# Kernel optimization log

Measured on AMD Instinct MI355X. Metric: run time of the kernel, lower is better.

## Reference

```python
import jax, jax.numpy as jnp
import numpy as np
import math

L = 32            # one_side_length; seq_len = L*L = 1024
EMBED = 768
NDIM = 16
N_SSM = 768
DIRS = 4
K = DIRS * N_SSM  # kernel_dim = 3072
REPEAT = EMBED // N_SSM
SCALE = math.sqrt(1.0 / NDIM)


def _compute_kernel(A_angle, A_radius, B1p, B2p, C1p, C2p):
    # Polar-parameterized complex diagonal A's (4 transition coeffs), sigmoid B, raw C.
    ang = jax.nn.sigmoid(A_angle) * (2.0 * math.pi)
    rad = jax.nn.sigmoid(A_radius)
    A = (rad * jnp.cos(ang) + 1j * (rad * jnp.sin(ang))).astype(jnp.complex64)  # (4,K,NDIM)
    A1, A2, A3, A4 = A[0], A[1], A[2], A[3]
    sB1 = jax.nn.sigmoid(B1p); sB2 = jax.nn.sigmoid(B2p)
    B1 = (sB1[..., 0] + 1j * sB1[..., 1]).astype(jnp.complex64)   # (K,NDIM)
    B2 = (sB2[..., 0] + 1j * sB2[..., 1]).astype(jnp.complex64)
    C1 = (C1p[..., 0] + 1j * C1p[..., 1]).astype(jnp.complex64)
    C2 = (C2p[..., 0] + 1j * C2p[..., 1]).astype(jnp.complex64)

    zeros = jnp.zeros((L, K, NDIM), jnp.complex64)

    # 2-D SSM impulse response (same math the torch module precomputes via the
    # vandermonde / coefficient-table expansion):
    #   x_h[i,j] = A1 x_h[i,j-1] + A2 x_v[i,j-1] + B1 delta[i,j]
    #   x_v[i,j] = A3 x_h[i-1,j] + A4 x_v[i-1,j] + B2 delta[i,j]
    #   k[i,j]   = scale * Re(C1 . x_h[i,j] + C2 . x_v[i,j])
    def row_step(carry, i):
        xh_prev, xv_prev = carry                    # row i-1 states, (L,K,NDIM)
        first = (i == 0).astype(jnp.float32)
        xv = A3 * xh_prev + A4 * xv_prev            # vertical flow from row above
        xv = xv.at[0].add(first * B2)               # impulse at (0,0)
        h0 = (first * B1).astype(jnp.complex64)     # x_h[i,0]
        def col_step(h, v_left):
            h_new = A1 * h + A2 * v_left            # horizontal flow within the row
            return h_new, h_new
        _, xh_rest = jax.lax.scan(col_step, h0, xv[:-1])
        xh = jnp.concatenate([h0[None], xh_rest], axis=0)
        return (xh, xv), (xh, xv)

    (_, _), (XH, XV) = jax.lax.scan(row_step, (zeros, zeros), jnp.arange(L))
    # XH, XV: (L, L, K, NDIM) complex
    k = SCALE * (jnp.einsum('ijhn,hn->ijh', XH, C1) + jnp.einsum('ijhn,hn->ijh', XV, C2))
    # boundary corrections exactly as in the torch module
    k = k.at[0, :, :].multiply(2.0)
    k = k.at[:, 0, :].multiply(2.0)
    k = k.at[0, 0, :].divide(4.0)
    return k.real                                   # (L, L, K) float32


def _forward(x, A_angle, A_radius, B1p, B2p, C1p, C2p, omega):
    S, B, D = x.shape
    residual = x * omega
    k = _compute_kernel(A_angle, A_radius, B1p, B2p, C1p, C2p)
    k = jnp.transpose(k, (2, 0, 1))                 # (K, L, L)
    x4 = jnp.transpose(x, (1, 2, 0)).reshape(B, D, L, L)
    s2 = (2 * L, 2 * L)
    flips = [(), (-2,), (-1,), (-2, -1)]
    out = jnp.zeros((B, D, L, L), jnp.float32)
    for idx, fl in enumerate(flips):                # 4 scan directions via flips
        kk = jnp.tile(k[idx * N_SSM:(idx + 1) * N_SSM], (REPEAT, 1, 1))  # (D,L,L)
        xc = jnp.flip(x4, axis=fl) if fl else x4
        kf = jnp.fft.rfft2(kk, s=s2)
        xf = jnp.fft.rfft2(xc, s=s2)
        cur = jnp.fft.irfft2(xf * kf, s=s2)[..., :L, :L]
        out = out + (jnp.flip(cur, axis=fl) if fl else cur)
    out = jnp.transpose(out.reshape(B, D, S), (2, 0, 1))  # back to (S,B,D)
    return jax.nn.silu(out + residual)


def setup_inputs() -> dict:
    key = jax.random.key(0)
    ks = jax.random.split(key, 9)
    x = jax.random.normal(ks[0], (L * L, 16, EMBED), jnp.float32)
    A_angle = jax.random.uniform(ks[1], (4, K, NDIM), jnp.float32, 0.5, 3.0)
    A_radius = jax.random.uniform(ks[2], (4, K, NDIM), jnp.float32, 0.5, 3.0)
    B1p = 0.2 * jax.random.normal(ks[3], (K, NDIM, 2), jnp.float32)
    B2p = 0.2 * jax.random.normal(ks[4], (K, NDIM, 2), jnp.float32)
    C1p = jax.random.normal(ks[5], (K, NDIM, 2), jnp.float32)
    C2p = jax.random.normal(ks[6], (K, NDIM, 2), jnp.float32)
    omega = jax.random.normal(ks[7], (EMBED,), jnp.float32)
    return {"x": x, "A_angle": A_angle, "A_radius": A_radius, "B1p": B1p,
            "B2p": B2p, "C1p": C1p, "C2p": C2p, "omega": omega}


def reference(x, A_angle, A_radius, B1p, B2p, C1p, C2p, omega):
    return _forward(x, A_angle, A_radius, B1p, B2p, C1p, C2p, omega)
```

## Files before the change

### kernel.cpp

```cpp
#include <hip/hip_runtime.h>
#include <cmath>

#define TWO_PI 6.283185307179586476925f

__device__ __forceinline__ float sigm(float v) { return 1.0f / (1.0f + expf(-v)); }
__device__ __forceinline__ float2 cadd(float2 a, float2 b) { return make_float2(a.x + b.x, a.y + b.y); }
__device__ __forceinline__ float2 csub(float2 a, float2 b) { return make_float2(a.x - b.x, a.y - b.y); }
__device__ __forceinline__ float2 cmulf(float2 a, float2 b) {
    return make_float2(a.x * b.x - a.y * b.y, a.x * b.y + a.y * b.x);
}

template<int CTRL>
__device__ __forceinline__ float dpp0(float v) {
    return __int_as_float(__builtin_amdgcn_update_dpp(
        0, __float_as_int(v), CTRL, 0xf, 0xf, true));
}
#define DPP_SHR1 0x111
#define DPP_SHR2 0x112
#define DPP_SHR4 0x114
#define DPP_ROR8 0x128

__device__ __forceinline__ float swz_xor16(float v) {
    return __int_as_float(__builtin_amdgcn_ds_swizzle(__float_as_int(v), 0x401F));
}

__device__ __forceinline__ int swz(int r, int c) {
    return (r << 6) | (c ^ ((r ^ (r << 3)) & 63));
}

__device__ __forceinline__ int gfidx(int o, int m, int c) {
    return o + (c << 3) + (m << 9);
}

template<bool INV, bool HALF, bool PRUNE>
__device__ __forceinline__ void dft8(float2* x) {
    const float RS = 0.70710678118654752440f;
    float2 t0, t1, t2, t3, t4, t5, t6, t7;
    if (HALF) {
        t0 = x[0]; t4 = x[0]; t1 = x[1]; t5 = x[1];
        t2 = x[2]; t6 = x[2]; t3 = x[3]; t7 = x[3];
    } else {
        t0 = cadd(x[0], x[4]); t4 = csub(x[0], x[4]);
        t1 = cadd(x[1], x[5]); t5 = csub(x[1], x[5]);
        t2 = cadd(x[2], x[6]); t6 = csub(x[2], x[6]);
        t3 = cadd(x[3], x[7]); t7 = csub(x[3], x[7]);
    }
    float2 t5w, t6w, t7w;
    if (!INV) {
        t5w = make_float2(RS * (t5.x + t5.y), RS * (t5.y - t5.x));
        t6w = make_float2(t6.y, -t6.x);
        t7w = make_float2(RS * (t7.y - t7.x), -RS * (t7.x + t7.y));
    } else {
        t5w = make_float2(RS * (t5.x - t5.y), RS * (t5.y + t5.x));
        t6w = make_float2(-t6.y, t6.x);
        t7w = make_float2(-RS * (t7.x + t7.y), RS * (t7.x - t7.y));
    }
    float2 u0 = cadd(t0, t2), u2 = csub(t0, t2), u1 = cadd(t1, t3), dd = csub(t1, t3);
    float2 u3 = INV ? make_float2(-dd.y, dd.x) : make_float2(dd.y, -dd.x);
    x[0] = cadd(u0, u1); x[2] = cadd(u2, u3);
    if (!PRUNE) { x[4] = csub(u0, u1); x[6] = csub(u2, u3); }
    float2 v0 = cadd(t4, t6w), v2 = csub(t4, t6w), v1 = cadd(t5w, t7w), ee = csub(t5w, t7w);
    float2 v3 = INV ? make_float2(-ee.y, ee.x) : make_float2(ee.y, -ee.x);
    x[1] = cadd(v0, v1); x[3] = cadd(v2, v3);
    if (!PRUNE) { x[5] = csub(v0, v1); x[7] = csub(v2, v3); }
}

__device__ __forceinline__ void make_tw(int o, float2* tw) {
    float s, co;
    sincosf(-TWO_PI * (float)o / 64.f, &s, &co);
    tw[0] = make_float2(co, s);
#pragma unroll
    for (int k = 1; k < 7; ++k) tw[k] = cmulf(tw[k - 1], tw[0]);
}

template<bool INV, bool COL, bool HALF, bool PRUNE>
__device__ __forceinline__ void fft64(float2* a, float2* r, const float2* tw,
                                      int o, int line) {
    dft8<INV, HALF, false>(r);
#pragma unroll
    for (int k = 1; k < 8; ++k) {
        float2 w = tw[k - 1];
        if (INV) w.y = -w.y;
        r[k] = cmulf(r[k], w);
    }
#pragma unroll
    for (int m = 0; m < 8; ++m) {
        int s = 8 * o + m;
        a[COL ? swz(s, line) : swz(line, s)] = r[m];
    }
#pragma unroll
    for (int j = 0; j < 8; ++j) {
        int s = 8 * j + o;
        r[j] = a[COL ? swz(s, line) : swz(line, s)];
    }
    dft8<INV, false, PRUNE>(r);
}

__global__ __launch_bounds__(512) void ssm_gf(
        const float* __restrict__ Aang, const float* __restrict__ Arad,
        const float* __restrict__ B1p, const float* __restrict__ B2p,
        const float* __restrict__ C1p, const float* __restrict__ C2p,
        float2* __restrict__ Gf) {
    __shared__ float2 a[4096];
    __shared__ float row0buf[4][2][64];
    __shared__ float col0buf[2][2][64];
    int d = blockIdx.x;
    int tid = threadIdx.x;
    int w = tid >> 6;
    int t = w & 3;
    int nh = w >> 2;
    int lane = tid & 63;
    int jg = lane & 7;
    int n8 = lane >> 3;
    int n = n8 + 8 * nh;
    int ch = t * 768 + d;
    int gid = ch * 16 + n;

    for (int e = tid; e < 4096; e += 512) a[e] = make_float2(0.f, 0.f);
    (&row0buf[0][0][0])[tid] = 0.f;
    if (tid < 256) (&col0buf[0][0][0])[tid] = 0.f;

    float ar[4], ai[4];
#pragma unroll
    for (int q = 0; q < 4; ++q) {
        float ang = sigm(Aang[q * 49152 + gid]) * TWO_PI;
        float rad = sigm(Arad[q * 49152 + gid]);
        float s, co;
        sincosf(ang, &s, &co);
        ar[q] = rad * co; ai[q] = rad * s;
    }
    float a1r = ar[0], a1i = ai[0], a2r = ar[1], a2i = ai[1];
    float a3r = ar[2], a3i = ai[2], a4r = ar[3], a4i = ai[3];
    float p2r = a1r * a1r - a1i * a1i, p2i = 2.f * a1r * a1i;
    float p3r = a1r * p2r - a1i * p2i, p3i = a1r * p2i + a1i * p2r;
    float p4r = p2r * p2r - p2i * p2i, p4i = 2.f * p2r * p2i;
    float p8r = p4r * p4r - p4i * p4i, p8i = 2.f * p4r * p4i;
    float p16r = p8r * p8r - p8i * p8i, p16i = 2.f * p8r * p8i;
    float cz1r = (jg >= 1) ? p4r : 0.f,  cz1i = (jg >= 1) ? p4i : 0.f;
    float cz2r = (jg >= 2) ? p8r : 0.f,  cz2i = (jg >= 2) ? p8i : 0.f;
    float cz4r = (jg >= 4) ? p16r : 0.f, cz4i = (jg >= 4) ? p16i : 0.f;

    const float2* B1v = (const float2*)B1p;
    const float2* B2v = (const float2*)B2p;
    const float2* C1v = (const float2*)C1p;
    const float2* C2v = (const float2*)C2p;
    float2 b1 = B1v[gid], b2 = B2v[gid], c1 = C1v[gid], c2 = C2v[gid];
    float b1r = sigm(b1.x), b1i = sigm(b1.y);
    float b2r = sigm(b2.x), b2i = sigm(b2.y);
    float c1r = c1.x, c1i = c1.y, c2r = c2.x, c2i = c2.y;

    float pwr = 1.f, pwi = 0.f;
    if (jg & 1) { pwr = p4r; pwi = p4i; }
    if (jg & 2) { float tr = pwr * p8r - pwi * p8i;  pwi = pwr * p8i + pwi * p8r;  pwr = tr; }
    if (jg & 4) { float tr = pwr * p16r - pwi * p16i; pwi = pwr * p16i + pwi * p16r; pwr = tr; }
    float ebr = pwr * b1r - pwi * b1i, ebi = pwr * b1i + pwi * b1r;

    int bb0 = n8 & 1, bb1 = (n8 >> 1) & 1;
    int col = 4 * jg + 2 * bb0 + bb1;
    int ccl = (t & 2) ? ((64 - col) & 63) : col;

    __syncthreads();

    float xvr[4], xvi[4], xhr[4], xhi[4];
#pragma unroll
    for (int m = 0; m < 4; ++m) { xvr[m] = 0.f; xvi[m] = 0.f; xhr[m] = 0.f; xhi[m] = 0.f; }

    auto body = [&](int i, bool is0) {
#pragma unroll
        for (int m = 0; m < 4; ++m) {
            float nr = a3r * xhr[m] - a3i * xhi[m] + a4r * xvr[m] - a4i * xvi[m];
            float ni = a3r * xhi[m] + a3i * xhr[m] + a4r * xvi[m] + a4i * xvr[m];
            xvr[m] = nr; xvi[m] = ni;
        }
        if (is0 && jg == 0) { xvr[0] += b2r; xvi[0] += b2i; }
        float g1r = a2r * xvr[0] - a2i * xvi[0];
        float g1i = a2r * xvi[0] + a2i * xvr[0];
        float g2r = a1r * g1r - a1i * g1i + a2r * xvr[1] - a2i * xvi[1];
        float g2i = a1r * g1i + a1i * g1r + a2r * xvi[1] + a2i * xvr[1];
        float g3r = a1r * g2r - a1i * g2i + a2r * xvr[2] - a2i * xvi[2];
        float g3i = a1r * g2i + a1i * g2r + a2r * xvi[2] + a2i * xvr[2];
        float ldr = a1r * g3r - a1i * g3i + a2r * xvr[3] - a2i * xvi[3];
        float ldi = a1r * g3i + a1i * g3r + a2r * xvi[3] + a2i * xvr[3];
        float Vr = ldr, Vi = ldi, sr, si;
        sr = dpp0<DPP_SHR1>(Vr); si = dpp0<DPP_SHR1>(Vi);
        Vr += cz1r * sr - cz1i * si; Vi += cz1r * si + cz1i * sr;
        sr = dpp0<DPP_SHR2>(Vr); si = dpp0<DPP_SHR2>(Vi);
        Vr += cz2r * sr - cz2i * si; Vi += cz2r * si + cz2i * sr;
        sr = dpp0<DPP_SHR4>(Vr); si = dpp0<DPP_SHR4>(Vi);
        Vr += cz4r * sr - cz4i * si; Vi += cz4r * si + cz4i * sr;
        float Er = dpp0<DPP_SHR1>(Vr), Ei = dpp0<DPP_SHR1>(Vi);
        Er = (jg == 0) ? 0.f : Er; Ei = (jg == 0) ? 0.f : Ei;
        if (is0) { Er += ebr; Ei += ebi; }
        xhr[0] = Er; xhi[0] = Ei;
        xhr[1] = a1r * Er - a1i * Ei + g1r;  xhi[1] = a1r * Ei + a1i * Er + g1i;
        xhr[2] = p2r * Er - p2i * Ei + g2r;  xhi[2] = p2r * Ei + p2i * Er + g2i;
        xhr[3] = p3r * Er - p3i * Ei + g3r;  xhi[3] = p3r * Ei + p3i * Er + g3i;
        float v0 = c1r * xhr[0] - c1i * xhi[0] + c2r * xvr[0] - c2i * xvi[0];
        float v1 = c1r * xhr[1] - c1i * xhi[1] + c2r * xvr[1] - c2i * xvi[1];
        float v2 = c1r * xhr[2] - c1i * xhi[2] + c2r * xvr[2] - c2i * xvi[2];
        float v3 = c1r * xhr[3] - c1i * xhi[3] + c2r * xvr[3] - c2i * xvi[3];
        float s0 = bb0 ? v0 : v2, s1 = bb0 ? v1 : v3;
        float r0 = dpp0<DPP_ROR8>(s0), r1 = dpp0<DPP_ROR8>(s1);
        float q0 = (bb0 ? v2 : v0) + r0;
        float q1 = (bb0 ? v3 : v1) + r1;
        float s2 = bb1 ? q0 : q1;
        float r2 = swz_xor16(s2);
        float qq = (bb1 ? q1 : q0) + r2;
        qq += __shfl_xor(qq, 32, 64);
        if (n8 < 4) {
            if (is0) {
                row0buf[t][nh][ccl] = qq;
            } else if (col == 0) {
                col0buf[t >> 1][nh][(t & 1) ? (64 - i) : i] = qq;
            } else {
                int rr_ = (t & 1) ? (64 - i) : i;
                ((float*)&a[swz(rr_, ccl)])[nh] = qq;
            }
        }
    };
    body(0, true);
#pragma unroll 1
    for (int i = 1; i < 32; ++i) body(i, false);

    __syncthreads();
    for (int e = tid; e < 4096; e += 512) {
        int r = e >> 6, cm = e & 63;
        int c = cm ^ ((r ^ (r << 3)) & 63);
        float2 cv = a[e];
        float v = cv.x + cv.y;
        if (r == 0) {
            v += row0buf[0][0][c] + row0buf[0][1][c] + row0buf[1][0][c] + row0buf[1][1][c]
               + row0buf[2][0][c] + row0buf[2][1][c] + row0buf[3][0][c] + row0buf[3][1][c];
        } else if (c == 0) {
            v += col0buf[0][0][r] + col0buf[0][1][r] + col0buf[1][0][r] + col0buf[1][1][r];
        }
        float f = 0.25f;
        if (r == 0) f *= 2.f;
        if (c == 0) f *= 2.f;
        if (r == 0 && c == 0) f *= 0.25f;
        a[e] = make_float2(f * v, 0.f);
    }
    __syncthreads();
    int o = tid & 7;
    float2 tw[7];
    make_tw(o, tw);
    {
        int row = tid >> 3;
        float2 r[8];
#pragma unroll
        for (int j = 0; j < 8; ++j) r[j] = a[swz(row, 8 * j + o)];
        fft64<false, false, false, false>(a, r, tw, o, row);
#pragma unroll
        for (int m = 0; m < 8; ++m) a[swz(row, o + 8 * m)] = r[m];
    }
    __syncthreads();
    {
        int cc = tid >> 3;
        float2 r[8];
#pragma unroll
        for (int j = 0; j < 8; ++j) r[j] = a[swz(8 * j + o, cc)];
        fft64<false, true, false, false>(a, r, tw, o, cc);
#pragma unroll
        for (int m = 0; m < 8; ++m) Gf[d * 4096 + gfidx(o, m, cc)] = r[m];
    }
}

__global__ __launch_bounds__(256) void transpose_in(const float* __restrict__ x,
                                                    float* __restrict__ xT) {
    __shared__ float t[64][65];
    int bR = blockIdx.x % 192, bS = blockIdx.x / 192;
    int r0 = bR * 64, s0 = bS * 64;
    int c = threadIdx.x & 63, w = threadIdx.x >> 6;
#pragma unroll
    for (int k = 0; k < 16; ++k) {
        int row = w + 4 * k;
        t[row][c] = x[(size_t)(s0 + row) * 12288 + r0 + c];
    }
    __syncthreads();
#pragma unroll
    for (int k = 0; k < 16; ++k) {
        int row = w + 4 * k;
        xT[(size_t)(r0 + row) * 1024 + s0 + c] = t[c][row];
    }
}

__global__ __launch_bounds__(256) void transpose_out(const float* __restrict__ xT,
                                                     float* __restrict__ out) {
    __shared__ float t[64][65];
    int bR = blockIdx.x % 192, bS = blockIdx.x / 192;
    int r0 = bR * 64, s0 = bS * 64;
    int c = threadIdx.x & 63, w = threadIdx.x >> 6;
#pragma unroll
    for (int k = 0; k < 16; ++k) {
        int row = w + 4 * k;
        t[row][c] = xT[(size_t)(r0 + row) * 1024 + s0 + c];
    }
    __syncthreads();
#pragma unroll
    for (int k = 0; k < 16; ++k) {
        int row = w + 4 * k;
        out[(size_t)(s0 + row) * 12288 + r0 + c] = t[c][row];
    }
}

__global__ __launch_bounds__(256) void conv_fft(
        const float* __restrict__ x, float* __restrict__ xT,
        const float2* __restrict__ Gf, const float* __restrict__ omega,
        float* __restrict__ out, int useT) {
    __shared__ float2 a[4096];
    int bid = (blockIdx.x & 7) * 768 + (blockIdx.x >> 3);
    int d = bid >> 3, b = (bid & 7) * 2;
    int tid = threadIdx.x;
    int o = tid & 7;
    float2 tw[7];
    make_tw(o, tw);
    const size_t base0 = (size_t)(b * 768 + d) * 1024;
    const size_t base1 = (size_t)((b + 1) * 768 + d) * 1024;
    {
        int row = tid >> 3;
        float2 r[8];
#pragma unroll
        for (int j = 0; j < 4; ++j) {
            int s2 = row * 32 + 8 * j + o;
            if (useT) r[j] = make_float2(xT[base0 + s2], xT[base1 + s2]);
            else      r[j] = make_float2(x[s2 * 12288 + b * 768 + d],
                                         x[s2 * 12288 + (b + 1) * 768 + d]);
        }
#pragma unroll
        for (int j = 4; j < 8; ++j) r[j] = make_float2(0.f, 0.f);
        fft64<false, false, true, false>(a, r, tw, o, row);
#pragma unroll
        for (int m = 0; m < 8; ++m) a[swz(row, o + 8 * m)] = r[m];
    }
    __syncthreads();
#pragma unroll 1
    for (int sw = 0; sw < 2; ++sw) {
        int c = sw * 32 + (tid >> 3);
        float2 r[8];
#pragma unroll
        for (int j = 0; j < 4; ++j) r[j] = a[swz(8 * j + o, c)];
#pragma unroll
        for (int j = 4; j < 8; ++j) r[j] = make_float2(0.f, 0.f);
        fft64<false, true, true, false>(a, r, tw, o, c);
#pragma unroll
        for (int m = 0; m < 8; ++m) {
            r[m] = cmulf(r[m], Gf[d * 4096 + gfidx(o, m, c)]);
        }
        fft64<true, true, false, true>(a, r, tw, o, c);
#pragma unroll
        for (int m = 0; m < 4; ++m) a[swz(o + 8 * m, c)] = r[m];
    }
    __syncthreads();
    {
        int row = tid >> 3;
        float2 r[8];
#pragma unroll
        for (int j = 0; j < 8; ++j) r[j] = a[swz(row, 8 * j + o)];
        fft64<true, false, false, true>(a, r, tw, o, row);
        float w = omega[d];
        const float inv = 1.0f / 4096.0f;
#pragma unroll
        for (int m = 0; m < 4; ++m) {
            int cc = o + 8 * m;
            int s2 = row * 32 + cc;
            float xa, xb;
            if (useT) { xa = xT[base0 + s2]; xb = xT[base1 + s2]; }
            else {
                xa = x[s2 * 12288 + b * 768 + d];
                xb = x[s2 * 12288 + (b + 1) * 768 + d];
            }
            float ya = r[m].x * inv + xa * w;
            float yb = r[m].y * inv + xb * w;
            float oa = ya / (1.0f + expf(-ya));
            float ob = yb / (1.0f + expf(-yb));
            if (useT) {
                xT[base0 + s2] = oa;
                xT[base1 + s2] = ob;
            } else {
                out[s2 * 12288 + b * 768 + d] = oa;
                out[s2 * 12288 + (b + 1) * 768 + d] = ob;
            }
        }
    }
}

extern "C" void kernel_launch(void* const* d_in, const int* in_sizes, int n_in,
                              void* d_out, int out_size, void* d_ws, size_t ws_size,
                              hipStream_t stream) {
    const float* x     = (const float*)d_in[0];
    const float* Aang  = (const float*)d_in[1];
    const float* Arad  = (const float*)d_in[2];
    const float* B1p   = (const float*)d_in[3];
    const float* B2p   = (const float*)d_in[4];
    const float* C1p   = (const float*)d_in[5];
    const float* C2p   = (const float*)d_in[6];
    const float* omega = (const float*)d_in[7];
    float* out = (float*)d_out;
    char* ws = (char*)d_ws;

    float2* Gf = (float2*)ws;
    float*  xT = (float*)(ws + 25165824);
    int useT = (ws_size >= (size_t)75497472) ? 1 : 0;

    ssm_gf<<<768, 512, 0, stream>>>(Aang, Arad, B1p, B2p, C1p, C2p, Gf);
    if (useT) transpose_in<<<3072, 256, 0, stream>>>(x, xT);
    conv_fft<<<6144, 256, 0, stream>>>(x, xT, Gf, omega, out, useT);
    if (useT) transpose_out<<<3072, 256, 0, stream>>>(xT, out);
}
```

Measured before the change: 168.3 us.

## Fuse input transpose into SSM kernel, widen conv blocks, use packed float2 math

Merges the input transpose into the SSM impulse/FFT kernel as extra blocks, so the two independent jobs run in one launch and can overlap. The conv FFT kernel moves to 512 threads, so the column pass covers all 64 columns in one sweep instead of two, while half the threads sit idle in the row passes. Complex arithmetic is rewritten with ext_vector float2 types so the compiler can emit packed FP32 instructions. Fast-math __expf and __sincosf replace the precise versions, which slightly loosens accuracy.

```diff
diff --git a/kernel.cpp b/kernel.cpp
--- a/kernel.cpp
+++ b/kernel.cpp
@@ -3,11 +3,13 @@
 
 #define TWO_PI 6.283185307179586476925f
 
-__device__ __forceinline__ float sigm(float v) { return 1.0f / (1.0f + expf(-v)); }
-__device__ __forceinline__ float2 cadd(float2 a, float2 b) { return make_float2(a.x + b.x, a.y + b.y); }
-__device__ __forceinline__ float2 csub(float2 a, float2 b) { return make_float2(a.x - b.x, a.y - b.y); }
-__device__ __forceinline__ float2 cmulf(float2 a, float2 b) {
-    return make_float2(a.x * b.x - a.y * b.y, a.x * b.y + a.y * b.x);
+typedef float f2 __attribute__((ext_vector_type(2)));
+
+__device__ __forceinline__ float sigm(float v) { return 1.0f / (1.0f + __expf(-v)); }
+__device__ __forceinline__ f2 mnegi(f2 v) { return (f2){v.y, -v.x}; }
+__device__ __forceinline__ f2 mposi(f2 v) { return (f2){-v.y, v.x}; }
+__device__ __forceinline__ f2 cmulf(f2 a, f2 b) {
+    return (f2){a.x, a.x} * b + (f2){a.y, a.y} * mposi(b);
 }
 
 template<int CTRL>
@@ -33,53 +35,53 @@
 }
 
 template<bool INV, bool HALF, bool PRUNE>
-__device__ __forceinline__ void dft8(float2* x) {
+__device__ __forceinline__ void dft8(f2* x) {
     const float RS = 0.70710678118654752440f;
-    float2 t0, t1, t2, t3, t4, t5, t6, t7;
+    f2 t0, t1, t2, t3, t4, t5, t6, t7;
     if (HALF) {
         t0 = x[0]; t4 = x[0]; t1 = x[1]; t5 = x[1];
         t2 = x[2]; t6 = x[2]; t3 = x[3]; t7 = x[3];
     } else {
-        t0 = cadd(x[0], x[4]); t4 = csub(x[0], x[4]);
-        t1 = cadd(x[1], x[5]); t5 = csub(x[1], x[5]);
-        t2 = cadd(x[2], x[6]); t6 = csub(x[2], x[6]);
-        t3 = cadd(x[3], x[7]); t7 = csub(x[3], x[7]);
-    }
-    float2 t5w, t6w, t7w;
+        t0 = x[0] + x[4]; t4 = x[0] - x[4];
+        t1 = x[1] + x[5]; t5 = x[1] - x[5];
+        t2 = x[2] + x[6]; t6 = x[2] - x[6];
+        t3 = x[3] + x[7]; t7 = x[3] - x[7];
+    }
+    f2 t5w, t6w, t7w;
     if (!INV) {
-        t5w = make_float2(RS * (t5.x + t5.y), RS * (t5.y - t5.x));
-        t6w = make_float2(t6.y, -t6.x);
-        t7w = make_float2(RS * (t7.y - t7.x), -RS * (t7.x + t7.y));
+        t5w = RS * (t5 + mnegi(t5));
+        t6w = mnegi(t6);
+        t7w = RS * (mnegi(t7) - t7);
     } else {
-        t5w = make_float2(RS * (t5.x - t5.y), RS * (t5.y + t5.x));
-        t6w = make_float2(-t6.y, t6.x);
-        t7w = make_float2(-RS * (t7.x + t7.y), RS * (t7.x - t7.y));
-    }
-    float2 u0 = cadd(t0, t2), u2 = csub(t0, t2), u1 = cadd(t1, t3), dd = csub(t1, t3);
-    float2 u3 = INV ? make_float2(-dd.y, dd.x) : make_float2(dd.y, -dd.x);
-    x[0] = cadd(u0, u1); x[2] = cadd(u2, u3);
-    if (!PRUNE) { x[4] = csub(u0, u1); x[6] = csub(u2, u3); }
-    float2 v0 = cadd(t4, t6w), v2 = csub(t4, t6w), v1 = cadd(t5w, t7w), ee = csub(t5w, t7w);
-    float2 v3 = INV ? make_float2(-ee.y, ee.x) : make_float2(ee.y, -ee.x);
-    x[1] = cadd(v0, v1); x[3] = cadd(v2, v3);
-    if (!PRUNE) { x[5] = csub(v0, v1); x[7] = csub(v2, v3); }
-}
-
-__device__ __forceinline__ void make_tw(int o, float2* tw) {
+        t5w = RS * (t5 - mnegi(t5));
+        t6w = mposi(t6);
+        t7w = RS * (mposi(t7) - t7);
+    }
+    f2 u0 = t0 + t2, u2 = t0 - t2, u1 = t1 + t3, dd = t1 - t3;
+    f2 u3 = INV ? mposi(dd) : mnegi(dd);
+    x[0] = u0 + u1; x[2] = u2 + u3;
+    if (!PRUNE) { x[4] = u0 - u1; x[6] = u2 - u3; }
+    f2 v0 = t4 + t6w, v2 = t4 - t6w, v1 = t5w + t7w, ee = t5w - t7w;
+    f2 v3 = INV ? mposi(ee) : mnegi(ee);
+    x[1] = v0 + v1; x[3] = v2 + v3;
+    if (!PRUNE) { x[5] = v0 - v1; x[7] = v2 - v3; }
+}
+
+__device__ __forceinline__ void make_tw(int o, f2* tw) {
     float s, co;
-    sincosf(-TWO_PI * (float)o / 64.f, &s, &co);
-    tw[0] = make_float2(co, s);
+    __sincosf(-TWO_PI * (float)o / 64.f, &s, &co);
+    tw[0] = (f2){co, s};
 #pragma unroll
     for (int k = 1; k < 7; ++k) tw[k] = cmulf(tw[k - 1], tw[0]);
 }
 
 template<bool INV, bool COL, bool HALF, bool PRUNE>
-__device__ __forceinline__ void fft64(float2* a, float2* r, const float2* tw,
+__device__ __forceinline__ void fft64(f2* a, f2* r, const f2* tw,
                                       int o, int line) {
     dft8<INV, HALF, false>(r);
 #pragma unroll
     for (int k = 1; k < 8; ++k) {
-        float2 w = tw[k - 1];
+        f2 w = tw[k - 1];
         if (INV) w.y = -w.y;
         r[k] = cmulf(r[k], w);
     }
@@ -96,16 +98,39 @@
     dft8<INV, false, PRUNE>(r);
 }
 
-__global__ __launch_bounds__(512) void ssm_gf(
+__global__ __launch_bounds__(512) void ssm_tin(
         const float* __restrict__ Aang, const float* __restrict__ Arad,
         const float* __restrict__ B1p, const float* __restrict__ B2p,
         const float* __restrict__ C1p, const float* __restrict__ C2p,
-        float2* __restrict__ Gf) {
-    __shared__ float2 a[4096];
-    __shared__ float row0buf[4][2][64];
-    __shared__ float col0buf[2][2][64];
+        f2* __restrict__ Gf, const float* __restrict__ x,
+        float* __restrict__ xT) {
+    __shared__ __align__(16) char smem[35840];
+    int tid = threadIdx.x;
+
+    if (blockIdx.x >= 768) {
+        float (*tt)[65] = (float (*)[65])smem;
+        int bb = blockIdx.x - 768;
+        int bR = bb % 192, bS = bb / 192;
+        int r0 = bR * 64, s0 = bS * 64;
+        int c = tid & 63, w = tid >> 6;
+#pragma unroll
+        for (int k = 0; k < 8; ++k) {
+            int row = w + 8 * k;
+            tt[row][c] = x[(size_t)(s0 + row) * 12288 + r0 + c];
+        }
+        __syncthreads();
+#pragma unroll
+        for (int k = 0; k < 8; ++k) {
+            int row = w + 8 * k;
+            xT[(size_t)(r0 + row) * 1024 + s0 + c] = tt[c][row];
+        }
+        return;
+    }
+
+    f2* a = (f2*)smem;
+    float* row0 = (float*)(smem + 32768);
+    float* col0 = (float*)(smem + 34816);
     int d = blockIdx.x;
-    int tid = threadIdx.x;
     int w = tid >> 6;
     int t = w & 3;
     int nh = w >> 2;
@@ -116,9 +141,9 @@
     int ch = t * 768 + d;
     int gid = ch * 16 + n;
 
-    for (int e = tid; e < 4096; e += 512) a[e] = make_float2(0.f, 0.f);
-    (&row0buf[0][0][0])[tid] = 0.f;
-    if (tid < 256) (&col0buf[0][0][0])[tid] = 0.f;
+    for (int e = tid; e < 4096; e += 512) a[e] = (f2){0.f, 0.f};
+    row0[tid] = 0.f;
+    if (tid < 256) col0[tid] = 0.f;
 
     float ar[4], ai[4];
 #pragma unroll
@@ -126,7 +151,7 @@
         float ang = sigm(Aang[q * 49152 + gid]) * TWO_PI;
         float rad = sigm(Arad[q * 49152 + gid]);
         float s, co;
-        sincosf(ang, &s, &co);
+        __sincosf(ang, &s, &co);
         ar[q] = rad * co; ai[q] = rad * s;
     }
     float a1r = ar[0], a1i = ai[0], a2r = ar[1], a2i = ai[1];
@@ -209,9 +234,9 @@
         qq += __shfl_xor(qq, 32, 64);
         if (n8 < 4) {
             if (is0) {
-                row0buf[t][nh][ccl] = qq;
+                row0[(((t << 1) | nh) << 6) | ccl] = qq;
             } else if (col == 0) {
-                col0buf[t >> 1][nh][(t & 1) ? (64 - i) : i] = qq;
+                col0[((((t >> 1) << 1) | nh) << 6) | ((t & 1) ? (64 - i) : i)] = qq;
             } else {
                 int rr_ = (t & 1) ? (64 - i) : i;
                 ((float*)&a[swz(rr_, ccl)])[nh] = qq;
@@ -226,27 +251,27 @@
     for (int e = tid; e < 4096; e += 512) {
         int r = e >> 6, cm = e & 63;
         int c = cm ^ ((r ^ (r << 3)) & 63);
-        float2 cv = a[e];
+        f2 cv = a[e];
         float v = cv.x + cv.y;
         if (r == 0) {
-            v += row0buf[0][0][c] + row0buf[0][1][c] + row0buf[1][0][c] + row0buf[1][1][c]
-               + row0buf[2][0][c] + row0buf[2][1][c] + row0buf[3][0][c] + row0buf[3][1][c];
+            v += row0[c] + row0[64 + c] + row0[128 + c] + row0[192 + c]
+               + row0[256 + c] + row0[320 + c] + row0[384 + c] + row0[448 + c];
         } else if (c == 0) {
-            v += col0buf[0][0][r] + col0buf[0][1][r] + col0buf[1][0][r] + col0buf[1][1][r];
+            v += col0[r] + col0[64 + r] + col0[128 + r] + col0[192 + r];
         }
         float f = 0.25f;
         if (r == 0) f *= 2.f;
         if (c == 0) f *= 2.f;
         if (r == 0 && c == 0) f *= 0.25f;
-        a[e] = make_float2(f * v, 0.f);
+        a[e] = (f2){f * v, 0.f};
     }
     __syncthreads();
     int o = tid & 7;
-    float2 tw[7];
+    f2 tw[7];
     make_tw(o, tw);
     {
         int row = tid >> 3;
-        float2 r[8];
+        f2 r[8];
 #pragma unroll
         for (int j = 0; j < 8; ++j) r[j] = a[swz(row, 8 * j + o)];
         fft64<false, false, false, false>(a, r, tw, o, row);
@@ -256,7 +281,7 @@
     __syncthreads();
     {
         int cc = tid >> 3;
-        float2 r[8];
+        f2 r[8];
 #pragma unroll
         for (int j = 0; j < 8; ++j) r[j] = a[swz(8 * j + o, cc)];
         fft64<false, true, false, false>(a, r, tw, o, cc);
@@ -265,82 +290,43 @@
     }
 }
 
-__global__ __launch_bounds__(256) void transpose_in(const float* __restrict__ x,
-                                                    float* __restrict__ xT) {
-    __shared__ float t[64][65];
-    int bR = blockIdx.x % 192, bS = blockIdx.x / 192;
-    int r0 = bR * 64, s0 = bS * 64;
-    int c = threadIdx.x & 63, w = threadIdx.x >> 6;
-#pragma unroll
-    for (int k = 0; k < 16; ++k) {
-        int row = w + 4 * k;
-        t[row][c] = x[(size_t)(s0 + row) * 12288 + r0 + c];
-    }
-    __syncthreads();
-#pragma unroll
-    for (int k = 0; k < 16; ++k) {
-        int row = w + 4 * k;
-        xT[(size_t)(r0 + row) * 1024 + s0 + c] = t[c][row];
-    }
-}
-
-__global__ __launch_bounds__(256) void transpose_out(const float* __restrict__ xT,
-                                                     float* __restrict__ out) {
-    __shared__ float t[64][65];
-    int bR = blockIdx.x % 192, bS = blockIdx.x / 192;
-    int r0 = bR * 64, s0 = bS * 64;
-    int c = threadIdx.x & 63, w = threadIdx.x >> 6;
-#pragma unroll
-    for (int k = 0; k < 16; ++k) {
-        int row = w + 4 * k;
-        t[row][c] = xT[(size_t)(r0 + row) * 1024 + s0 + c];
-    }
-    __syncthreads();
-#pragma unroll
-    for (int k = 0; k < 16; ++k) {
-        int row = w + 4 * k;
-        out[(size_t)(s0 + row) * 12288 + r0 + c] = t[c][row];
-    }
-}
-
-__global__ __launch_bounds__(256) void conv_fft(
+__global__ __launch_bounds__(512) void conv_fft(
         const float* __restrict__ x, float* __restrict__ xT,
-        const float2* __restrict__ Gf, const float* __restrict__ omega,
+        const f2* __restrict__ Gf, const float* __restrict__ omega,
         float* __restrict__ out, int useT) {
-    __shared__ float2 a[4096];
+    __shared__ f2 a[4096];
     int bid = (blockIdx.x & 7) * 768 + (blockIdx.x >> 3);
     int d = bid >> 3, b = (bid & 7) * 2;
     int tid = threadIdx.x;
-    int o = tid & 7;
-    float2 tw[7];
+    int o = tid & 7, grp = tid >> 3;
+    f2 tw[7];
     make_tw(o, tw);
     const size_t base0 = (size_t)(b * 768 + d) * 1024;
     const size_t base1 = (size_t)((b + 1) * 768 + d) * 1024;
-    {
-        int row = tid >> 3;
-        float2 r[8];
+    if (grp < 32) {
+        int row = grp;
+        f2 r[8];
 #pragma unroll
         for (int j = 0; j < 4; ++j) {
             int s2 = row * 32 + 8 * j + o;
-            if (useT) r[j] = make_float2(xT[base0 + s2], xT[base1 + s2]);
-            else      r[j] = make_float2(x[s2 * 12288 + b * 768 + d],
-                                         x[s2 * 12288 + (b + 1) * 768 + d]);
-        }
-#pragma unroll
-        for (int j = 4; j < 8; ++j) r[j] = make_float2(0.f, 0.f);
+            if (useT) r[j] = (f2){xT[base0 + s2], xT[base1 + s2]};
+            else      r[j] = (f2){x[s2 * 12288 + b * 768 + d],
+                                  x[s2 * 12288 + (b + 1) * 768 + d]};
+        }
+#pragma unroll
+        for (int j = 4; j < 8; ++j) r[j] = (f2){0.f, 0.f};
         fft64<false, false, true, false>(a, r, tw, o, row);
 #pragma unroll
         for (int m = 0; m < 8; ++m) a[swz(row, o + 8 * m)] = r[m];
     }
     __syncthreads();
-#pragma unroll 1
-    for (int sw = 0; sw < 2; ++sw) {
-        int c = sw * 32 + (tid >> 3);
-        float2 r[8];
+    {
+        int c = grp;
+        f2 r[8];
 #pragma unroll
         for (int j = 0; j < 4; ++j) r[j] = a[swz(8 * j + o, c)];
 #pragma unroll
-        for (int j = 4; j < 8; ++j) r[j] = make_float2(0.f, 0.f);
+        for (int j = 4; j < 8; ++j) r[j] = (f2){0.f, 0.f};
         fft64<false, true, true, false>(a, r, tw, o, c);
 #pragma unroll
         for (int m = 0; m < 8; ++m) {
@@ -351,9 +337,9 @@
         for (int m = 0; m < 4; ++m) a[swz(o + 8 * m, c)] = r[m];
     }
     __syncthreads();
-    {
-        int row = tid >> 3;
-        float2 r[8];
+    if (grp < 32) {
+        int row = grp;
+        f2 r[8];
 #pragma unroll
         for (int j = 0; j < 8; ++j) r[j] = a[swz(row, 8 * j + o)];
         fft64<true, false, false, true>(a, r, tw, o, row);
@@ -371,8 +357,8 @@
             }
             float ya = r[m].x * inv + xa * w;
             float yb = r[m].y * inv + xb * w;
-            float oa = ya / (1.0f + expf(-ya));
-            float ob = yb / (1.0f + expf(-yb));
+            float oa = ya / (1.0f + __expf(-ya));
+            float ob = yb / (1.0f + __expf(-yb));
             if (useT) {
                 xT[base0 + s2] = oa;
                 xT[base1 + s2] = ob;
@@ -381,6 +367,25 @@
                 out[s2 * 12288 + (b + 1) * 768 + d] = ob;
             }
         }
+    }
+}
+
+__global__ __launch_bounds__(256) void transpose_out(const float* __restrict__ xT,
+                                                     float* __restrict__ out) {
+    __shared__ float t[64][65];
+    int bR = blockIdx.x % 192, bS = blockIdx.x / 192;
+    int r0 = bR * 64, s0 = bS * 64;
+    int c = threadIdx.x & 63, w = threadIdx.x >> 6;
+#pragma unroll
+    for (int k = 0; k < 16; ++k) {
+        int row = w + 4 * k;
+        t[row][c] = xT[(size_t)(r0 + row) * 1024 + s0 + c];
+    }
+    __syncthreads();
+#pragma unroll
+    for (int k = 0; k < 16; ++k) {
+        int row = w + 4 * k;
+        out[(size_t)(s0 + row) * 12288 + r0 + c] = t[c][row];
     }
 }
 
@@ -398,12 +403,12 @@
     float* out = (float*)d_out;
     char* ws = (char*)d_ws;
 
-    float2* Gf = (float2*)ws;
-    float*  xT = (float*)(ws + 25165824);
+    f2*    Gf = (f2*)ws;
+    float* xT = (float*)(ws + 25165824);
     int useT = (ws_size >= (size_t)75497472) ? 1 : 0;
 
-    ssm_gf<<<768, 512, 0, stream>>>(Aang, Arad, B1p, B2p, C1p, C2p, Gf);
-    if (useT) transpose_in<<<3072, 256, 0, stream>>>(x, xT);
-    conv_fft<<<6144, 256, 0, stream>>>(x, xT, Gf, omega, out, useT);
+    int grid1 = useT ? 3840 : 768;
+    ssm_tin<<<grid1, 512, 0, stream>>>(Aang, Arad, B1p, B2p, C1p, C2p, Gf, x, xT);
+    conv_fft<<<6144, 512, 0, stream>>>(x, xT, Gf, omega, out, useT);
     if (useT) transpose_out<<<3072, 256, 0, stream>>>(xT, out);
 }
```

New measurement: 153.7 us. -8.7%, faster.
